# Kernel tuning notes

Hardware: AMD Instinct MI355X
Metric: run time of the kernel (lower is better)

The kernel has to match this reference:

```python
import jax, jax.numpy as jnp
import numpy as np

N_WG = 512      # waveguides n
N_COL = 512     # mesh columns
M = N_WG // 2   # node slots per column (odd columns have one masked dummy)
N_NODE = N_COL * M
B = 8192        # batch of input fields
PI4 = np.pi / 4


def build_mesh_indices():
    """Rectangular (Clements-style) mesh: per-column (top, bottom, mask) arrays."""
    top = np.zeros((N_COL, M), np.int32)
    bottom = np.zeros((N_COL, M), np.int32)
    mask = np.zeros((N_COL, M), np.int32)
    for c in range(N_COL):
        if c % 2 == 0:
            t = np.arange(0, N_WG, 2, dtype=np.int32)
            top[c], bottom[c], mask[c] = t, t + 1, 1
        else:
            t = np.arange(1, N_WG - 1, 2, dtype=np.int32)
            k = len(t)
            top[c, :k], bottom[c, :k], mask[c, :k] = t, t + 1, 1
            # masked dummy slot uses otherwise-unused rows 0 and N_WG-1
            top[c, k:], bottom[c, k:] = 0, N_WG - 1
    return jnp.asarray(top), jnp.asarray(bottom), jnp.asarray(mask)


def setup_inputs() -> dict:
    key = jax.random.key(0)
    ks = jax.random.split(key, 6)
    top, bottom, mask = build_mesh_indices()
    return {
        "x": jax.random.normal(ks[0], (N_WG, B), dtype=jnp.float32),
        "thetas": 2 * np.pi * jax.random.uniform(ks[1], (N_NODE,), dtype=jnp.float32),
        "phis": 2 * np.pi * jax.random.uniform(ks[2], (N_NODE,), dtype=jnp.float32),
        "gammas": 2 * np.pi * jax.random.uniform(ks[3], (N_WG,), dtype=jnp.float32),
        "bs_errors": 0.01 * jax.random.normal(ks[4], (N_NODE, 2), dtype=jnp.float32),
        "loss_errors": -0.1 * jax.random.uniform(ks[5], (N_NODE, 2), dtype=jnp.float32),
        "top": top, "bottom": bottom, "mask": mask,
    }


def _dc_terms(bs_errors, loss_errors, side):
    """_parallel_dc: per-node directional-coupler 2x2 elements [N,4] complex."""
    ins = jnp.exp(jnp.log(10.0) * loss_errors[:, side] / 20.0)
    e = bs_errors[:, side]
    s, c = jnp.sin(PI4 + e), jnp.cos(PI4 + e)
    t11 = (ins * s).astype(jnp.complex64)
    t12 = ins * (1j * c)
    t21 = (1j * c).astype(jnp.complex64)
    t22 = s.astype(jnp.complex64)
    return jnp.stack([t11, t12, t21, t22], axis=-1)


def _transform(v, T, t, b, m):
    """_parallel_transform: masked 2x2 gather-multiply-scatter. T: [M,4] complex."""
    vt, vb = v[t], v[b]
    one_m = 1.0 - m
    s11 = (T[:, 0] * m + one_m)[:, None]
    s12 = (T[:, 1] * m)[:, None]
    s21 = (T[:, 2] * m)[:, None]
    s22 = (T[:, 3] * m + one_m)[:, None]
    return v.at[t].set(s11 * vt + s21 * vb).at[b].set(s12 * vt + s22 * vb)


def reference(x, thetas, phis, gammas, bs_errors, loss_errors, top, bottom, mask):
    # input gamma phase screen, then propagate through all mesh columns
    v = x.astype(jnp.complex64) * jnp.exp(1j * gammas)[:, None]          # [n, B]
    left = _dc_terms(bs_errors, loss_errors, 0).reshape(N_COL, M, 4)
    right = _dc_terms(bs_errors, loss_errors, 1).reshape(N_COL, M, 4)
    th = thetas.reshape(N_COL, M)
    ph = phis.reshape(N_COL, M)
    mf = mask.astype(jnp.float32)

    def column(v, xs):
        t, b, m, thc, phc, L, R = xs
        # PhaseStyle.TOP, forward: phi -> left DC -> theta -> right DC
        v = v.at[t].multiply(jnp.exp(1j * phc * m)[:, None])
        v = _transform(v, L, t, b, m)
        v = v.at[t].multiply(jnp.exp(1j * thc * m)[:, None])
        v = _transform(v, R, t, b, m)
        return v, None

    v, _ = jax.lax.scan(column, v, (top, bottom, mf, th, ph, left, right))
    return jnp.stack([v.real, v.imag])  # [2, n, B]
```

## Files before the change

### kernel.cpp

```cpp
#include <hip/hip_runtime.h>
#include <math.h>

#define BATCH 8192
#define NROW 512
#define NCOL 512
#define MNODE 256

typedef __attribute__((ext_vector_type(8))) short bf16x8;
typedef __attribute__((ext_vector_type(4))) float f32x4;

__device__ __forceinline__ short2 split1(float x) {
  unsigned u = __float_as_uint(x);
  short h = (short)(u >> 16);
  float r = x - __uint_as_float(u & 0xffff0000u);
  short l = (short)(__float_as_uint(r) >> 16);
  return make_short2(h, l);
}

__global__ __launch_bounds__(256) void precomp_kernel(
    const float* __restrict__ thetas, const float* __restrict__ phis,
    const float* __restrict__ bse, const float* __restrict__ lse,
    float4* __restrict__ pp) {
  int n = blockIdx.x * 256 + threadIdx.x;
  float th = thetas[n], ph = phis[n];
  float e0 = bse[2 * n + 0], e1 = bse[2 * n + 1];
  float l0 = lse[2 * n + 0], l1 = lse[2 * n + 1];
  const float K = 0.16609640474436813f;
  float ins0 = exp2f(l0 * K), ins1 = exp2f(l1 * K);
  const float PI4 = 0.7853981633974483f;
  float s0, c0, s1, c1, sp, cp, st, ct;
  sincosf(PI4 + e0, &s0, &c0);
  sincosf(PI4 + e1, &s1, &c1);
  sincosf(ph, &sp, &cp);
  sincosf(th, &st, &ct);
  float AL = ins0 * s0, C1L = c0, C2L = ins0 * c0, SL = s0;
  float AR = ins1 * s1, C1R = c1, C2R = ins1 * c1, SR = s1;
  float a11r = AL * cp,   a11i = AL * sp;
  float a12r = 0.f,       a12i = C1L;
  float a21r = -C2L * sp, a21i = C2L * cp;
  float a22r = SL,        a22i = 0.f;
  float b11r = a11r * ct - a11i * st, b11i = a11r * st + a11i * ct;
  float b12r = a12r * ct - a12i * st, b12i = a12r * st + a12i * ct;
  float n11r = AR * b11r - C1R * a21i;
  float n11i = AR * b11i + C1R * a21r;
  float n12r = AR * b12r - C1R * a22i;
  float n12i = AR * b12i + C1R * a22r;
  float n21r = -C2R * b11i + SR * a21r;
  float n21i =  C2R * b11r + SR * a21i;
  float n22r = -C2R * b12i + SR * a22r;
  float n22i =  C2R * b12r + SR * a22i;
  pp[2 * n + 0] = make_float4(n11r, n11i, n12r, n12i);
  pp[2 * n + 1] = make_float4(n21r, n21i, n22r, n22i);
}

__device__ __forceinline__ void proc_pair(float& vtr, float& vti, float& vbr, float& vbi,
                                          const float4 q0, const float4 q1) {
  float tr = q0.x * vtr - q0.y * vti + q0.z * vbr - q0.w * vbi;
  float ti = q0.x * vti + q0.y * vtr + q0.z * vbi + q0.w * vbr;
  float br = q1.x * vtr - q1.y * vti + q1.z * vbr - q1.w * vbi;
  float bi = q1.x * vti + q1.y * vtr + q1.z * vbi + q1.w * vbr;
  vtr = tr; vti = ti; vbr = br; vbi = bi;
}

__device__ __forceinline__ int swz(int b) { return b ^ ((b >> 3) & 7); }

__global__ __launch_bounds__(256) void compose_kernel(
    const float* __restrict__ gammas, const float4* __restrict__ pp,
    float* __restrict__ Tsegs, int pairs_per_seg) {
  __shared__ float4 buf[2][1024];
  __shared__ float ep[1024][5];

  const int tid  = threadIdx.x;
  const int lane = tid & 63;
  const int w    = tid >> 6;
  const int seg  = blockIdx.x >> 7;
  const int g    = blockIdx.x & 127;
  const int col  = g * 4 + w;
  const int colmin = g * 4;

  const float4* ps = pp + (size_t)seg * pairs_per_seg * 1024;
  float* T = Tsegs + (size_t)seg * (1024 * NROW);

  float vr[8], vi[8];
#pragma unroll
  for (int r = 0; r < 8; ++r) {
    const int row = lane * 8 + r;
    vr[r] = 0.f; vi[r] = 0.f;
    if (row == col) {
      if (seg == 0) {
        float sg, cg;
        sincosf(gammas[row], &sg, &cg);
        vr[r] = cg; vi[r] = sg;
      } else {
        vr[r] = 1.f;
      }
    }
  }

  {
    const int sw = swz(tid);
#pragma unroll
    for (int k = 0; k < 4; ++k)
      buf[0][256 * k + sw] = ps[256 * k + tid];
  }
  __syncthreads();

  const int Lc = col >> 3;

#pragma unroll 1
  for (int p = 0; p < pairs_per_seg; ++p) {
    const int b = p & 1;

    const int HA = (p >> 2) + 3;
    const bool act  = (lane >= Lc - HA)     && (lane <= Lc + HA);
    const bool wide = (lane >= Lc - HA - 1) && (lane <= Lc + HA + 1);

    float4 f0, f1, f2, f3;
    bool st0 = false, st1 = false;
    if (p < pairs_per_seg - 1) {
      const int slo = colmin - 2 * p - 50;
      const int shi = colmin + 2 * p + 53;
      st0 = (tid + 1 >= slo) && (tid <= shi);
      st1 = (tid + 257 >= slo) && (tid + 256 <= shi);
      const float4* src = ps + (size_t)(p + 1) * 1024;
      if (st0) { f0 = src[tid];       f2 = src[512 + tid]; }
      if (st1) { f1 = src[256 + tid]; f3 = src[768 + tid]; }
    }

    float4 pe[8], po[7], pu1;
    if (act) {
      const int base = 8 * lane;
      const int l7 = lane & 7;
#pragma unroll
      for (int j = 0; j < 8; ++j) pe[j] = buf[b][base + (j ^ l7)];
#pragma unroll
      for (int j = 0; j < 7; ++j) po[j] = buf[b][512 + base + (j ^ l7)];
      const int lm = (lane == 0) ? 0 : lane - 1;
      pu1 = buf[b][512 + 8 * lm + (7 ^ (lm & 7))];

#pragma unroll
      for (int k = 0; k < 4; ++k)
        proc_pair(vr[2 * k], vi[2 * k], vr[2 * k + 1], vi[2 * k + 1],
                  pe[2 * k], pe[2 * k + 1]);

#pragma unroll
      for (int k = 0; k < 3; ++k)
        proc_pair(vr[2 * k + 1], vi[2 * k + 1], vr[2 * k + 2], vi[2 * k + 2],
                  po[2 * k], po[2 * k + 1]);
    }

    float br = 0.f, bi = 0.f, tu = 0.f, tv = 0.f;
    if (wide) {
      br = __shfl_down(vr[0], 1, 64);
      bi = __shfl_down(vi[0], 1, 64);
      tu = __shfl_up(vr[7], 1, 64);
      tv = __shfl_up(vi[7], 1, 64);
    }
    if (act) {
      float nAr = po[6].x * vr[7] - po[6].y * vi[7] + po[6].z * br - po[6].w * bi;
      float nAi = po[6].x * vi[7] + po[6].y * vr[7] + po[6].z * bi + po[6].w * br;
      float nBr = pu1.x * tu - pu1.y * tv + pu1.z * vr[0] - pu1.w * vi[0];
      float nBi = pu1.x * tv + pu1.y * tu + pu1.z * vi[0] + pu1.w * vr[0];
      if (lane < 63) { vr[7] = nAr; vi[7] = nAi; }
      if (lane > 0)  { vr[0] = nBr; vi[0] = nBi; }
    }

    if (p < pairs_per_seg - 1) {
      const int sw = swz(tid);
      if (st0) { buf[1 - b][sw] = f0;       buf[1 - b][512 + sw] = f2; }
      if (st1) { buf[1 - b][256 + sw] = f1; buf[1 - b][768 + sw] = f3; }
    }
    __syncthreads();
  }

#pragma unroll
  for (int r = 0; r < 8; ++r) {
    ep[lane * 8 + r][w] = vr[r];
    ep[512 + lane * 8 + r][w] = vi[r];
  }
  __syncthreads();
#pragma unroll
  for (int k = 0; k < 4; ++k) {
    const int i = k * 256 + tid;
    *(float4*)(T + (size_t)i * NROW + g * 4) =
        make_float4(ep[i][0], ep[i][1], ep[i][2], ep[i][3]);
  }
}

__global__ __launch_bounds__(256) void merge_mfma(
    const float* __restrict__ A0, const float* __restrict__ B0, float* __restrict__ C0,
    const float* __restrict__ A1, const float* __restrict__ B1, float* __restrict__ C1) {
  const float* A = blockIdx.z ? A1 : A0;
  const float* B = blockIdx.z ? B1 : B0;
  float*       C = blockIdx.z ? C1 : C0;

  __shared__ short sAh[64 * 40], sAl[64 * 40];

  const int tid = threadIdx.x;
  const int lane = tid & 63;
  const int w = tid >> 6;
  const int bm = blockIdx.y * 64;
  const int bn = blockIdx.x * 64;
  const int wm = (w & 1) * 32;
  const int wn = (w >> 1) * 32;
  const int q = lane >> 4;
  const int l15 = lane & 15;

  const int sm = tid >> 2;
  const int sk = (tid & 3) * 8;

  f32x4 acc[2][2];
#pragma unroll
  for (int i = 0; i < 2; ++i)
#pragma unroll
    for (int j = 0; j < 2; ++j) acc[i][j] = (f32x4){0.f, 0.f, 0.f, 0.f};

#pragma unroll 1
  for (int k0 = 0; k0 < 1024; k0 += 32) {
    {
      const int gm = bm + sm;
      const int gk = k0 + sk;
      const int r = gm & 511;
      const bool top = gm < 512;
      const bool left = gk < 512;
      const int col = gk & 511;
      const float* src = (top == left) ? (A + (size_t)r * 512)
                                       : (A + (size_t)(512 + r) * 512);
      const float sgn = (top && !left) ? -1.f : 1.f;
      float4 v0 = *(const float4*)(src + col);
      float4 v1 = *(const float4*)(src + col + 4);
      float vv[8] = {v0.x, v0.y, v0.z, v0.w, v1.x, v1.y, v1.z, v1.w};
      short h[8], l[8];
#pragma unroll
      for (int i = 0; i < 8; ++i) {
        short2 s = split1(sgn * vv[i]);
        h[i] = s.x; l[i] = s.y;
      }
      __syncthreads();
      *(bf16x8*)&sAh[sm * 40 + sk] = *(bf16x8*)h;
      *(bf16x8*)&sAl[sm * 40 + sk] = *(bf16x8*)l;
      __syncthreads();
    }

    bf16x8 bh[2], bl[2];
#pragma unroll
    for (int nt = 0; nt < 2; ++nt) {
      const float* bp = B + (size_t)(k0 + q * 8) * 512 + bn + wn + nt * 16 + l15;
      short hh[8], ll[8];
#pragma unroll
      for (int j = 0; j < 8; ++j) {
        short2 s = split1(bp[(size_t)j * 512]);
        hh[j] = s.x; ll[j] = s.y;
      }
      bh[nt] = *(bf16x8*)hh;
      bl[nt] = *(bf16x8*)ll;
    }

    bf16x8 ah[2], al[2];
#pragma unroll
    for (int mt = 0; mt < 2; ++mt) {
      const int m = wm + mt * 16 + l15;
      ah[mt] = *(const bf16x8*)&sAh[m * 40 + q * 8];
      al[mt] = *(const bf16x8*)&sAl[m * 40 + q * 8];
    }

#pragma unroll
    for (int mt = 0; mt < 2; ++mt)
#pragma unroll
      for (int nt = 0; nt < 2; ++nt) {
        acc[mt][nt] = __builtin_amdgcn_mfma_f32_16x16x32_bf16(ah[mt], bh[nt], acc[mt][nt], 0, 0, 0);
        acc[mt][nt] = __builtin_amdgcn_mfma_f32_16x16x32_bf16(ah[mt], bl[nt], acc[mt][nt], 0, 0, 0);
        acc[mt][nt] = __builtin_amdgcn_mfma_f32_16x16x32_bf16(al[mt], bh[nt], acc[mt][nt], 0, 0, 0);
      }
  }

#pragma unroll
  for (int mt = 0; mt < 2; ++mt)
#pragma unroll
    for (int nt = 0; nt < 2; ++nt)
#pragma unroll
      for (int r = 0; r < 4; ++r) {
        const int gm = bm + wm + mt * 16 + q * 4 + r;
        const int gn = bn + wn + nt * 16 + l15;
        C[(size_t)gm * 512 + gn] = acc[mt][nt][r];
      }
}

__global__ __launch_bounds__(256) void gemm_mfma(
    const float* __restrict__ A, const float* __restrict__ B,
    float* __restrict__ C) {
  __shared__ short sAh[128 * 40], sAl[128 * 40];

  const int tid = threadIdx.x;
  const int lane = tid & 63;
  const int w = tid >> 6;
  const int bm = blockIdx.y * 128;
  const int bn = blockIdx.x * 128;
  const int wm = (w & 1) * 64;
  const int wn = (w >> 1) * 64;
  const int q = lane >> 4;
  const int l15 = lane & 15;

  const int sm = tid >> 1;
  const int sk = (tid & 1) * 16;
  const float* Ap = A + (size_t)(bm + sm) * 512 + sk;

  f32x4 acc[4][4];
#pragma unroll
  for (int i = 0; i < 4; ++i)
#pragma unroll
    for (int j = 0; j < 4; ++j) acc[i][j] = (f32x4){0.f, 0.f, 0.f, 0.f};

  float4 pa[4];
#pragma unroll
  for (int i = 0; i < 4; ++i) pa[i] = *(const float4*)(Ap + i * 4);

#pragma unroll 1
  for (int k0 = 0; k0 < 512; k0 += 32) {
    {
      short h[16], l[16];
#pragma unroll
      for (int i = 0; i < 16; ++i) {
        short2 s = split1(((const float*)pa)[i]);
        h[i] = s.x; l[i] = s.y;
      }
      __syncthreads();
      *(bf16x8*)&sAh[sm * 40 + sk]     = *(bf16x8*)&h[0];
      *(bf16x8*)&sAh[sm * 40 + sk + 8] = *(bf16x8*)&h[8];
      *(bf16x8*)&sAl[sm * 40 + sk]     = *(bf16x8*)&l[0];
      *(bf16x8*)&sAl[sm * 40 + sk + 8] = *(bf16x8*)&l[8];
      __syncthreads();
    }

    if (k0 + 32 < 512) {
#pragma unroll
      for (int i = 0; i < 4; ++i) pa[i] = *(const float4*)(Ap + k0 + 32 + i * 4);
    }

    bf16x8 bh[4], bl[4];
#pragma unroll
    for (int nt = 0; nt < 4; ++nt) {
      const float* bp = B + (size_t)(k0 + q * 8) * BATCH + bn + wn + nt * 16 + l15;
      short hh[8], ll[8];
#pragma unroll
      for (int j = 0; j < 8; ++j) {
        short2 s = split1(bp[(size_t)j * BATCH]);
        hh[j] = s.x; ll[j] = s.y;
      }
      bh[nt] = *(bf16x8*)hh;
      bl[nt] = *(bf16x8*)ll;
    }

    bf16x8 ah[4], al[4];
#pragma unroll
    for (int mt = 0; mt < 4; ++mt) {
      const int m = wm + mt * 16 + l15;
      ah[mt] = *(const bf16x8*)&sAh[m * 40 + q * 8];
      al[mt] = *(const bf16x8*)&sAl[m * 40 + q * 8];
    }

#pragma unroll
    for (int mt = 0; mt < 4; ++mt)
#pragma unroll
      for (int nt = 0; nt < 4; ++nt) {
        acc[mt][nt] = __builtin_amdgcn_mfma_f32_16x16x32_bf16(ah[mt], bh[nt], acc[mt][nt], 0, 0, 0);
        acc[mt][nt] = __builtin_amdgcn_mfma_f32_16x16x32_bf16(ah[mt], bl[nt], acc[mt][nt], 0, 0, 0);
        acc[mt][nt] = __builtin_amdgcn_mfma_f32_16x16x32_bf16(al[mt], bh[nt], acc[mt][nt], 0, 0, 0);
      }
  }

#pragma unroll
  for (int mt = 0; mt < 4; ++mt)
#pragma unroll
    for (int nt = 0; nt < 4; ++nt)
#pragma unroll
      for (int r = 0; r < 4; ++r) {
        const int gm = bm + wm + mt * 16 + q * 4 + r;
        const int gn = bn + wn + nt * 16 + l15;
        C[(size_t)gm * BATCH + gn] = acc[mt][nt][r];
      }
}

extern "C" void kernel_launch(void* const* d_in, const int* in_sizes, int n_in,
                              void* d_out, int out_size, void* d_ws, size_t ws_size,
                              hipStream_t stream) {
  const float* x      = (const float*)d_in[0];
  const float* thetas = (const float*)d_in[1];
  const float* phis   = (const float*)d_in[2];
  const float* gammas = (const float*)d_in[3];
  const float* bse    = (const float*)d_in[4];
  const float* lse    = (const float*)d_in[5];

  float* base = (float*)d_ws;
  float4* pp  = (float4*)d_ws;
  const size_t PPF   = 1048576;
  const size_t SEGSZ = 524288;

  int nseg;
  if (ws_size >= (size_t)14 * 1024 * 1024)      nseg = 4;
  else if (ws_size >= (size_t)8 * 1024 * 1024)  nseg = 2;
  else                                          nseg = 1;

  float* segs = base + PPF;
  float* Tf;

  precomp_kernel<<<512, 256, 0, stream>>>(thetas, phis, bse, lse, pp);
  compose_kernel<<<nseg * 128, 256, 0, stream>>>(gammas, pp, segs, 256 / nseg);

  if (nseg == 4) {
    float* T0  = segs + 0 * SEGSZ;
    float* T1  = segs + 1 * SEGSZ;
    float* T2  = segs + 2 * SEGSZ;
    float* T3  = segs + 3 * SEGSZ;
    float* T10 = base;
    float* T32 = base + SEGSZ;
    Tf = segs + 4 * SEGSZ;
    merge_mfma<<<dim3(8, 16, 2), 256, 0, stream>>>(T1, T0, T10, T3, T2, T32);
    merge_mfma<<<dim3(8, 16, 1), 256, 0, stream>>>(T32, T10, Tf, T32, T10, Tf);
  } else if (nseg == 2) {
    float* T0 = segs + 0 * SEGSZ;
    float* T1 = segs + 1 * SEGSZ;
    Tf = base;
    merge_mfma<<<dim3(8, 16, 1), 256, 0, stream>>>(T1, T0, Tf, T1, T0, Tf);
  } else {
    Tf = segs;
  }

  gemm_mfma<<<dim3(BATCH / 128, 8), 256, 0, stream>>>(Tf, x, (float*)d_out);
}
```

Measured before the change: 260.1 us.

## Read compose coefficients directly from global memory and split mesh into eight segments

The compose kernel no longer stages per-column coefficients through a double-buffered LDS array with per-iteration barriers; each active lane loads its float4 coefficients straight from global memory, relying on cache. When the workspace is large enough, the mesh is split into eight segments instead of four, doubling compose parallelism and shortening each block's serial column chain, at the cost of an extra tree level of MFMA matrix merges. Without barriers, waves progress independently, but global load latency now sits on the serial dependency path.

New measurement: 349.9 us. +34.5%, slower.

```diff
diff --git a/kernel.cpp b/kernel.cpp
--- a/kernel.cpp
+++ b/kernel.cpp
@@ -62,12 +62,9 @@
   vtr = tr; vti = ti; vbr = br; vbi = bi;
 }
 
-__device__ __forceinline__ int swz(int b) { return b ^ ((b >> 3) & 7); }
-
 __global__ __launch_bounds__(256) void compose_kernel(
     const float* __restrict__ gammas, const float4* __restrict__ pp,
     float* __restrict__ Tsegs, int pairs_per_seg) {
-  __shared__ float4 buf[2][1024];
   __shared__ float ep[1024][5];
 
   const int tid  = threadIdx.x;
@@ -76,7 +73,6 @@
   const int seg  = blockIdx.x >> 7;
   const int g    = blockIdx.x & 127;
   const int col  = g * 4 + w;
-  const int colmin = g * 4;
 
   const float4* ps = pp + (size_t)seg * pairs_per_seg * 1024;
   float* T = Tsegs + (size_t)seg * (1024 * NROW);
@@ -97,46 +93,23 @@
     }
   }
 
-  {
-    const int sw = swz(tid);
-#pragma unroll
-    for (int k = 0; k < 4; ++k)
-      buf[0][256 * k + sw] = ps[256 * k + tid];
-  }
-  __syncthreads();
-
   const int Lc = col >> 3;
 
 #pragma unroll 1
   for (int p = 0; p < pairs_per_seg; ++p) {
-    const int b = p & 1;
-
     const int HA = (p >> 2) + 3;
     const bool act  = (lane >= Lc - HA)     && (lane <= Lc + HA);
     const bool wide = (lane >= Lc - HA - 1) && (lane <= Lc + HA + 1);
 
-    float4 f0, f1, f2, f3;
-    bool st0 = false, st1 = false;
-    if (p < pairs_per_seg - 1) {
-      const int slo = colmin - 2 * p - 50;
-      const int shi = colmin + 2 * p + 53;
-      st0 = (tid + 1 >= slo) && (tid <= shi);
-      st1 = (tid + 257 >= slo) && (tid + 256 <= shi);
-      const float4* src = ps + (size_t)(p + 1) * 1024;
-      if (st0) { f0 = src[tid];       f2 = src[512 + tid]; }
-      if (st1) { f1 = src[256 + tid]; f3 = src[768 + tid]; }
-    }
-
     float4 pe[8], po[7], pu1;
     if (act) {
-      const int base = 8 * lane;
-      const int l7 = lane & 7;
-#pragma unroll
-      for (int j = 0; j < 8; ++j) pe[j] = buf[b][base + (j ^ l7)];
-#pragma unroll
-      for (int j = 0; j < 7; ++j) po[j] = buf[b][512 + base + (j ^ l7)];
+      const float4* rowp = ps + (size_t)p * 1024 + 8 * lane;
+#pragma unroll
+      for (int j = 0; j < 8; ++j) pe[j] = rowp[j];
+#pragma unroll
+      for (int j = 0; j < 7; ++j) po[j] = rowp[512 + j];
       const int lm = (lane == 0) ? 0 : lane - 1;
-      pu1 = buf[b][512 + 8 * lm + (7 ^ (lm & 7))];
+      pu1 = ps[(size_t)p * 1024 + 512 + 8 * lm + 7];
 
 #pragma unroll
       for (int k = 0; k < 4; ++k)
@@ -164,13 +137,6 @@
       if (lane < 63) { vr[7] = nAr; vi[7] = nAi; }
       if (lane > 0)  { vr[0] = nBr; vi[0] = nBi; }
     }
-
-    if (p < pairs_per_seg - 1) {
-      const int sw = swz(tid);
-      if (st0) { buf[1 - b][sw] = f0;       buf[1 - b][512 + sw] = f2; }
-      if (st1) { buf[1 - b][256 + sw] = f1; buf[1 - b][768 + sw] = f3; }
-    }
-    __syncthreads();
   }
 
 #pragma unroll
@@ -397,7 +363,8 @@
   const size_t SEGSZ = 524288;
 
   int nseg;
-  if (ws_size >= (size_t)14 * 1024 * 1024)      nseg = 4;
+  if (ws_size >= (size_t)24 * 1024 * 1024)      nseg = 8;
+  else if (ws_size >= (size_t)14 * 1024 * 1024) nseg = 4;
   else if (ws_size >= (size_t)8 * 1024 * 1024)  nseg = 2;
   else                                          nseg = 1;
 
@@ -407,7 +374,21 @@
   precomp_kernel<<<512, 256, 0, stream>>>(thetas, phis, bse, lse, pp);
   compose_kernel<<<nseg * 128, 256, 0, stream>>>(gammas, pp, segs, 256 / nseg);
 
-  if (nseg == 4) {
+  if (nseg == 8) {
+    float* T[8];
+    for (int s = 0; s < 8; ++s) T[s] = segs + (size_t)s * SEGSZ;
+    float* T10 = base;
+    float* T32 = base + SEGSZ;
+    float* T54 = segs + 8 * SEGSZ;
+    float* T76 = segs + 9 * SEGSZ;
+    merge_mfma<<<dim3(8, 16, 2), 256, 0, stream>>>(T[1], T[0], T10, T[3], T[2], T32);
+    merge_mfma<<<dim3(8, 16, 2), 256, 0, stream>>>(T[5], T[4], T54, T[7], T[6], T76);
+    float* T3210 = segs;
+    float* T7654 = segs + SEGSZ;
+    merge_mfma<<<dim3(8, 16, 2), 256, 0, stream>>>(T32, T10, T3210, T76, T54, T7654);
+    Tf = base;
+    merge_mfma<<<dim3(8, 16, 1), 256, 0, stream>>>(T7654, T3210, Tf, T7654, T3210, Tf);
+  } else if (nseg == 4) {
     float* T0  = segs + 0 * SEGSZ;
     float* T1  = segs + 1 * SEGSZ;
     float* T2  = segs + 2 * SEGSZ;
```

## Pre-split input into packed bf16 hi/lo tiles and use packed final GEMM

Applied to the files above, without the earlier changes.

When the workspace is large enough, a new kernel splits x into bf16 hi/lo parts once, laid out in MFMA-fragment-ready packed order. A new final GEMM loads B fragments directly from global memory, so it no longer stages or re-splits B in shared memory, and it uses a 64x128 tile to launch more blocks. This removes the repeated per-block splitting of x. The cost is an extra kernel pass and extra workspace traffic, and the path is taken only when ws_size is at least 24MB.

Measured after the change: 266.8 us. 1.03x slower.

```diff
diff --git a/kernel.cpp b/kernel.cpp
--- a/kernel.cpp
+++ b/kernel.cpp
@@ -286,6 +286,112 @@
       }
 }
 
+__global__ __launch_bounds__(256) void xprep_kernel(
+    const float* __restrict__ x, short* __restrict__ xp) {
+  const int t = blockIdx.x * 256 + threadIdx.x;
+  const int n = t & 8191;
+  const int g = t >> 13;
+  const float* src = x + (size_t)g * 8 * BATCH + n;
+  short h[8], l[8];
+#pragma unroll
+  for (int j = 0; j < 8; ++j) {
+    short2 s = split1(src[(size_t)j * BATCH]);
+    h[j] = s.x; l[j] = s.y;
+  }
+  short* dst = xp + (size_t)t * 16;
+  *(bf16x8*)dst = *(bf16x8*)h;
+  *(bf16x8*)(dst + 8) = *(bf16x8*)l;
+}
+
+__global__ __launch_bounds__(256) void gemm_mfma_packed(
+    const float* __restrict__ A, const short* __restrict__ xp,
+    float* __restrict__ C) {
+  __shared__ short sAh[64 * 40], sAl[64 * 40];
+
+  const int tid = threadIdx.x;
+  const int lane = tid & 63;
+  const int w = tid >> 6;
+  const int bm = blockIdx.y * 64;
+  const int bn = blockIdx.x * 128;
+  const int wm = (w & 1) * 32;
+  const int wn = (w >> 1) * 64;
+  const int q = lane >> 4;
+  const int l15 = lane & 15;
+
+  const int sm = tid >> 2;
+  const int sk = (tid & 3) * 8;
+  const float* Ap = A + (size_t)(bm + sm) * 512 + sk;
+
+  f32x4 acc[2][4];
+#pragma unroll
+  for (int i = 0; i < 2; ++i)
+#pragma unroll
+    for (int j = 0; j < 4; ++j) acc[i][j] = (f32x4){0.f, 0.f, 0.f, 0.f};
+
+  float4 pa[2];
+  pa[0] = *(const float4*)(Ap);
+  pa[1] = *(const float4*)(Ap + 4);
+
+#pragma unroll 1
+  for (int k0 = 0; k0 < 512; k0 += 32) {
+    {
+      short h[8], l[8];
+#pragma unroll
+      for (int i = 0; i < 8; ++i) {
+        short2 s = split1(((const float*)pa)[i]);
+        h[i] = s.x; l[i] = s.y;
+      }
+      __syncthreads();
+      *(bf16x8*)&sAh[sm * 40 + sk] = *(bf16x8*)h;
+      *(bf16x8*)&sAl[sm * 40 + sk] = *(bf16x8*)l;
+      __syncthreads();
+    }
+
+    if (k0 + 32 < 512) {
+      pa[0] = *(const float4*)(Ap + k0 + 32);
+      pa[1] = *(const float4*)(Ap + k0 + 36);
+    }
+
+    const int kt = k0 >> 5;
+    bf16x8 bh[4], bl[4];
+#pragma unroll
+    for (int nt = 0; nt < 4; ++nt) {
+      const short* bp = xp + (((size_t)(kt * 4 + q)) * BATCH +
+                              (bn + wn + nt * 16 + l15)) * 16;
+      bh[nt] = *(const bf16x8*)bp;
+      bl[nt] = *(const bf16x8*)(bp + 8);
+    }
+
+    bf16x8 ah[2], al[2];
+#pragma unroll
+    for (int mt = 0; mt < 2; ++mt) {
+      const int m = wm + mt * 16 + l15;
+      ah[mt] = *(const bf16x8*)&sAh[m * 40 + q * 8];
+      al[mt] = *(const bf16x8*)&sAl[m * 40 + q * 8];
+    }
+
+#pragma unroll
+    for (int mt = 0; mt < 2; ++mt)
+#pragma unroll
+      for (int nt = 0; nt < 4; ++nt) {
+        acc[mt][nt] = __builtin_amdgcn_mfma_f32_16x16x32_bf16(ah[mt], bh[nt], acc[mt][nt], 0, 0, 0);
+        acc[mt][nt] = __builtin_amdgcn_mfma_f32_16x16x32_bf16(ah[mt], bl[nt], acc[mt][nt], 0, 0, 0);
+        acc[mt][nt] = __builtin_amdgcn_mfma_f32_16x16x32_bf16(al[mt], bh[nt], acc[mt][nt], 0, 0, 0);
+      }
+  }
+
+#pragma unroll
+  for (int mt = 0; mt < 2; ++mt)
+#pragma unroll
+    for (int nt = 0; nt < 4; ++nt)
+#pragma unroll
+      for (int r = 0; r < 4; ++r) {
+        const int gm = bm + wm + mt * 16 + q * 4 + r;
+        const int gn = bn + wn + nt * 16 + l15;
+        C[(size_t)gm * BATCH + gn] = acc[mt][nt][r];
+      }
+}
+
 __global__ __launch_bounds__(256) void gemm_mfma(
     const float* __restrict__ A, const float* __restrict__ B,
     float* __restrict__ C) {
@@ -396,35 +502,55 @@
   const size_t PPF   = 1048576;
   const size_t SEGSZ = 524288;
 
-  int nseg;
-  if (ws_size >= (size_t)14 * 1024 * 1024)      nseg = 4;
-  else if (ws_size >= (size_t)8 * 1024 * 1024)  nseg = 2;
-  else                                          nseg = 1;
-
-  float* segs = base + PPF;
-  float* Tf;
-
   precomp_kernel<<<512, 256, 0, stream>>>(thetas, phis, bse, lse, pp);
-  compose_kernel<<<nseg * 128, 256, 0, stream>>>(gammas, pp, segs, 256 / nseg);
-
-  if (nseg == 4) {
+
+  if (ws_size >= (size_t)24 * 1024 * 1024) {
+    float* segs = base + PPF;
+    compose_kernel<<<512, 256, 0, stream>>>(gammas, pp, segs, 64);
+
     float* T0  = segs + 0 * SEGSZ;
     float* T1  = segs + 1 * SEGSZ;
     float* T2  = segs + 2 * SEGSZ;
     float* T3  = segs + 3 * SEGSZ;
-    float* T10 = base;
-    float* T32 = base + SEGSZ;
-    Tf = segs + 4 * SEGSZ;
+    float* T10 = segs + 4 * SEGSZ;
+    float* T32 = segs + 5 * SEGSZ;
+    float* Tf  = base;
     merge_mfma<<<dim3(8, 16, 2), 256, 0, stream>>>(T1, T0, T10, T3, T2, T32);
     merge_mfma<<<dim3(8, 16, 1), 256, 0, stream>>>(T32, T10, Tf, T32, T10, Tf);
-  } else if (nseg == 2) {
-    float* T0 = segs + 0 * SEGSZ;
-    float* T1 = segs + 1 * SEGSZ;
-    Tf = base;
-    merge_mfma<<<dim3(8, 16, 1), 256, 0, stream>>>(T1, T0, Tf, T1, T0, Tf);
+
+    short* xp = (short*)(base + SEGSZ);
+    xprep_kernel<<<2048, 256, 0, stream>>>(x, xp);
+
+    gemm_mfma_packed<<<dim3(64, 16), 256, 0, stream>>>(Tf, xp, (float*)d_out);
   } else {
-    Tf = segs;
-  }
-
-  gemm_mfma<<<dim3(BATCH / 128, 8), 256, 0, stream>>>(Tf, x, (float*)d_out);
-}
+    int nseg;
+    if (ws_size >= (size_t)14 * 1024 * 1024)      nseg = 4;
+    else if (ws_size >= (size_t)8 * 1024 * 1024)  nseg = 2;
+    else                                          nseg = 1;
+
+    float* segs = base + PPF;
+    float* Tf;
+    compose_kernel<<<nseg * 128, 256, 0, stream>>>(gammas, pp, segs, 256 / nseg);
+
+    if (nseg == 4) {
+      float* T0  = segs + 0 * SEGSZ;
+      float* T1  = segs + 1 * SEGSZ;
+      float* T2  = segs + 2 * SEGSZ;
+      float* T3  = segs + 3 * SEGSZ;
+      float* T10 = base;
+      float* T32 = base + SEGSZ;
+      Tf = segs + 4 * SEGSZ;
+      merge_mfma<<<dim3(8, 16, 2), 256, 0, stream>>>(T1, T0, T10, T3, T2, T32);
+      merge_mfma<<<dim3(8, 16, 1), 256, 0, stream>>>(T32, T10, Tf, T32, T10, Tf);
+    } else if (nseg == 2) {
+      float* T0 = segs + 0 * SEGSZ;
+      float* T1 = segs + 1 * SEGSZ;
+      Tf = base;
+      merge_mfma<<<dim3(8, 16, 1), 256, 0, stream>>>(T1, T0, Tf, T1, T0, Tf);
+    } else {
+      Tf = segs;
+    }
+
+    gemm_mfma<<<dim3(BATCH / 128, 8), 256, 0, stream>>>(Tf, x, (float*)d_out);
+  }
+}
```
